# Kernel tuning notes

Hardware: AMD Instinct MI355X
Metric: run time of the kernel (lower is better)

The kernel has to match this reference:

```python
import jax, jax.numpy as jnp
import numpy as np

DIM_IN = 64
DIM_OUT = 64
SCALE = DIM_IN ** (-0.5)

def setup_inputs() -> dict:
    key = jax.random.key(0)
    ks = jax.random.split(key, 9)
    B, C, N, S = 4, DIM_IN, 16384, 16
    inp = {
        "xyz": jax.random.normal(ks[0], (B, 3, N), jnp.float32),
        "neighbor_xyz": jax.random.normal(ks[1], (B, 3, N, S), jnp.float32),
        "point": jax.random.normal(ks[2], (B, C, N), jnp.float32),
        "neighbor_points": jax.random.normal(ks[3], (B, C, N, S), jnp.float32),
        "neighbor_cost": jax.random.normal(ks[4], (B, C, N, S), jnp.float32),
        # 1x1 conv weights (kernel dims squeezed): [out_ch, in_ch]
        "w_k": jax.random.normal(ks[5], (DIM_IN, DIM_IN), jnp.float32) * (DIM_IN ** -0.5),
        "w_v": jax.random.normal(ks[6], (DIM_OUT, DIM_IN), jnp.float32) * (DIM_IN ** -0.5),
        "w_pos": jax.random.normal(ks[7], (DIM_IN, 4), jnp.float32) * 0.5,
        "b_pos": jax.random.normal(ks[8], (DIM_IN,), jnp.float32) * 0.01,
    }
    return inp

def reference(xyz, neighbor_xyz, point, neighbor_points, neighbor_cost, w_k, w_v, w_pos, b_pos):
    # xyz: [B,3,N]; neighbor_xyz: [B,3,N,S]; point: [B,C,N]; neighbor_cost: [B,C,N,S]
    tmp = xyz[:, :, :, None] - neighbor_xyz                      # [B,3,N,S]
    xyz_norm = jnp.linalg.norm(tmp, axis=1, keepdims=True)       # [B,1,N,S]
    pos = jnp.concatenate([tmp, xyz_norm], axis=1)               # [B,4,N,S]
    pos_enc = jnp.einsum('oc,bcns->bons', w_pos, pos) + b_pos[None, :, None, None]
    k = jnp.einsum('oc,bcns->bons', w_k, neighbor_cost + pos_enc)  # [B,C,N,S]
    v = jnp.einsum('oc,bcns->bons', w_v, neighbor_cost)            # [B,Co,N,S]
    q = point * SCALE                                              # note: self.q conv unused in original
    attn = jnp.einsum('bcn,bcns->bns', q, k)                       # channel-reduced scores
    attn = jax.nn.softmax(attn, axis=-1)                           # softmax over S neighbors
    out = jnp.einsum('bns,bcns->bcn', attn, v)                     # [B,Co,N]
    return out
```

## Files before the change

kernel.cpp:

```cpp
#include <hip/hip_runtime.h>

#define NCH    64
#define NPTS   16384
#define NS     16
#define QSCALE 0.125f

__global__ __launch_bounds__(256) void pt_attn_kernel(
    const float* __restrict__ xyz,
    const float* __restrict__ nxyz,
    const float* __restrict__ point,
    const float* __restrict__ cost,
    const float* __restrict__ w_k,
    const float* __restrict__ w_v,
    const float* __restrict__ w_pos,
    const float* __restrict__ b_pos,
    float* __restrict__ out)
{
    __shared__ float ptwc[NCH][64];
    __shared__ float qp[NCH][64];
    __shared__ float qg[5][64];

    const int t  = threadIdx.x;
    const int b  = blockIdx.x >> 8;
    const int n0 = (blockIdx.x & 255) << 6;

    const float* point_b = point + (size_t)b * NCH * NPTS;
    const float* cost_b  = cost  + (size_t)b * NCH * NPTS * NS;
    const float* xyz_b   = xyz   + (size_t)b * 3 * NPTS;
    const float* nxyz_b  = nxyz  + (size_t)b * 3 * NPTS * NS;
    float*       out_b   = out   + (size_t)b * NCH * NPTS;

    const int wu   = __builtin_amdgcn_readfirstlane(t >> 6);
    const int lane = t & 63;

#pragma unroll
    for (int i = 0; i < 4; ++i) {
        int o = wu * 4 + i;
        ptwc[o][lane] = point_b[o * NPTS + n0 + lane] * QSCALE;
    }
#pragma unroll
    for (int i = 4; i < 16; ++i) {
        int o = wu * 4 + (i & 3) + (i >> 2) * 16;
        ptwc[o][lane] = point_b[o * NPTS + n0 + lane] * QSCALE;
    }
    __syncthreads();

    {
        const int cbase = wu * 16;
        float acc[16];
#pragma unroll
        for (int j = 0; j < 16; ++j) acc[j] = 0.f;
#pragma unroll 4
        for (int o = 0; o < NCH; ++o) {
            float pv = ptwc[o][lane];
            const float* wkr = w_k + o * NCH + cbase;
#pragma unroll
            for (int j = 0; j < 16; ++j)
                acc[j] = fmaf(wkr[j], pv, acc[j]);
        }
#pragma unroll
        for (int j = 0; j < 16; ++j)
            qp[cbase + j][lane] = acc[j];
    }
    __syncthreads();

    {
        const int j = wu;
        float a = 0.f, ab = 0.f;
#pragma unroll 8
        for (int c = 0; c < NCH; ++c) {
            float q = qp[c][lane];
            a = fmaf(q, w_pos[c * 4 + j], a);
            if (j == 0) ab = fmaf(q, b_pos[c], ab);
        }
        qg[j][lane] = a;
        if (j == 0) qg[4][lane] = ab;
    }
    __syncthreads();

    const int s4 = t & 3, nl = t >> 2;
    const int n  = n0 + nl;
    const float4* costp = (const float4*)(cost_b + (size_t)n * NS) + s4;

    float4 lg;
    {
        float x0 = xyz_b[0 * NPTS + n];
        float x1 = xyz_b[1 * NPTS + n];
        float x2 = xyz_b[2 * NPTS + n];
        float4 a0 = *(const float4*)(nxyz_b + (size_t)(0 * NPTS + n) * NS + s4 * 4);
        float4 a1 = *(const float4*)(nxyz_b + (size_t)(1 * NPTS + n) * NS + s4 * 4);
        float4 a2 = *(const float4*)(nxyz_b + (size_t)(2 * NPTS + n) * NS + s4 * 4);
        float qs0 = qg[0][nl], qs1 = qg[1][nl], qs2 = qg[2][nl];
        float qs3 = qg[3][nl], qb  = qg[4][nl];
        float t0, t1, t2, nr;
        t0 = x0 - a0.x; t1 = x1 - a1.x; t2 = x2 - a2.x;
        nr = sqrtf(fmaf(t0, t0, fmaf(t1, t1, t2 * t2)));
        lg.x = fmaf(qs0, t0, fmaf(qs1, t1, fmaf(qs2, t2, fmaf(qs3, nr, qb))));
        t0 = x0 - a0.y; t1 = x1 - a1.y; t2 = x2 - a2.y;
        nr = sqrtf(fmaf(t0, t0, fmaf(t1, t1, t2 * t2)));
        lg.y = fmaf(qs0, t0, fmaf(qs1, t1, fmaf(qs2, t2, fmaf(qs3, nr, qb))));
        t0 = x0 - a0.z; t1 = x1 - a1.z; t2 = x2 - a2.z;
        nr = sqrtf(fmaf(t0, t0, fmaf(t1, t1, t2 * t2)));
        lg.z = fmaf(qs0, t0, fmaf(qs1, t1, fmaf(qs2, t2, fmaf(qs3, nr, qb))));
        t0 = x0 - a0.w; t1 = x1 - a1.w; t2 = x2 - a2.w;
        nr = sqrtf(fmaf(t0, t0, fmaf(t1, t1, t2 * t2)));
        lg.w = fmaf(qs0, t0, fmaf(qs1, t1, fmaf(qs2, t2, fmaf(qs3, nr, qb))));
    }

#pragma unroll 8
    for (int c = 0; c < NCH; ++c) {
        float4 cv = costp[(size_t)c * NPTS * 4];
        float qc = qp[c][nl];
        lg.x = fmaf(qc, cv.x, lg.x);
        lg.y = fmaf(qc, cv.y, lg.y);
        lg.z = fmaf(qc, cv.z, lg.z);
        lg.w = fmaf(qc, cv.w, lg.w);
    }

    float m = fmaxf(fmaxf(lg.x, lg.y), fmaxf(lg.z, lg.w));
    m = fmaxf(m, __shfl_xor(m, 1));
    m = fmaxf(m, __shfl_xor(m, 2));
    float4 at;
    at.x = __expf(lg.x - m);
    at.y = __expf(lg.y - m);
    at.z = __expf(lg.z - m);
    at.w = __expf(lg.w - m);
    float Z = at.x + at.y + at.z + at.w;
    Z += __shfl_xor(Z, 1);
    Z += __shfl_xor(Z, 2);
    float rz = 1.f / Z;
    at.x *= rz; at.y *= rz; at.z *= rz; at.w *= rz;

#pragma unroll 8
    for (int c = 0; c < NCH; ++c) {
        float4 cv = costp[(size_t)c * NPTS * 4];
        float p = fmaf(at.x, cv.x, fmaf(at.y, cv.y, fmaf(at.z, cv.z, at.w * cv.w)));
        p += __shfl_xor(p, 1);
        p += __shfl_xor(p, 2);
        if (s4 == 0) ptwc[c][nl] = p;
    }
    __syncthreads();

    {
        const int obase = wu * 16;
        float acc[16];
#pragma unroll
        for (int j = 0; j < 16; ++j) acc[j] = 0.f;
#pragma unroll 4
        for (int c = 0; c < NCH; ++c) {
            float wv = ptwc[c][lane];
            const float* wvc = w_v + c;
#pragma unroll
            for (int j = 0; j < 16; ++j)
                acc[j] = fmaf(wvc[(obase + j) * NCH], wv, acc[j]);
        }
#pragma unroll
        for (int j = 0; j < 16; ++j)
            out_b[(obase + j) * NPTS + n0 + lane] = acc[j];
    }
}

extern "C" void kernel_launch(void* const* d_in, const int* in_sizes, int n_in,
                              void* d_out, int out_size, void* d_ws, size_t ws_size,
                              hipStream_t stream) {
    const float* xyz   = (const float*)d_in[0];
    const float* nxyz  = (const float*)d_in[1];
    const float* point = (const float*)d_in[2];
    const float* cost  = (const float*)d_in[4];
    const float* w_k   = (const float*)d_in[5];
    const float* w_v   = (const float*)d_in[6];
    const float* w_pos = (const float*)d_in[7];
    const float* b_pos = (const float*)d_in[8];
    float* outp = (float*)d_out;

    dim3 grid(1024), block(256);
    hipLaunchKernelGGL(pt_attn_kernel, grid, block, 0, stream,
                       xyz, nxyz, point, cost, w_k, w_v, w_pos, b_pos, outp);
}
```

Measured before the change: 535.2 us.

## Shrink point tile to 16 and cache cost tile in registers

Cuts the per-block point tile from 64 to 16 and launches four times as many blocks. Each thread now loads its share of the cost tensor into registers once and reuses it for both the logit and the weighted-sum passes, where before it read cost from global memory twice. The two weight matrices are staged in padded shared memory and the small channel matvecs use float4 LDS reads. In exchange, every block reloads both full 64x64 weight matrices, syncs more often, and holds 64 extra registers for the cost tile, which could limit occupancy.

After: 498.2 us. -6.9%, faster.

```diff
diff --git a/kernel.cpp b/kernel.cpp
--- a/kernel.cpp
+++ b/kernel.cpp
@@ -5,7 +5,7 @@
 #define NS     16
 #define QSCALE 0.125f
 
-__global__ __launch_bounds__(256) void pt_attn_kernel(
+__global__ __launch_bounds__(256, 4) void pt_attn_kernel(
     const float* __restrict__ xyz,
     const float* __restrict__ nxyz,
     const float* __restrict__ point,
@@ -16,13 +16,17 @@
     const float* __restrict__ b_pos,
     float* __restrict__ out)
 {
-    __shared__ float ptwc[NCH][64];
-    __shared__ float qp[NCH][64];
-    __shared__ float qg[5][64];
+    __shared__ float wmat[64][68];
+    __shared__ float ptq[64][16];
+    __shared__ float qp[16][68];
+    __shared__ float wpb[5][65];
+    __shared__ float qg[5][16];
+    __shared__ float linit[4][64];
+    __shared__ float wc[16][68];
 
     const int t  = threadIdx.x;
-    const int b  = blockIdx.x >> 8;
-    const int n0 = (blockIdx.x & 255) << 6;
+    const int b  = blockIdx.x >> 10;
+    const int n0 = (blockIdx.x & 1023) << 4;
 
     const float* point_b = point + (size_t)b * NCH * NPTS;
     const float* cost_b  = cost  + (size_t)b * NCH * NPTS * NS;
@@ -30,133 +34,145 @@
     const float* nxyz_b  = nxyz  + (size_t)b * 3 * NPTS * NS;
     float*       out_b   = out   + (size_t)b * NCH * NPTS;
 
-    const int wu   = __builtin_amdgcn_readfirstlane(t >> 6);
+    const int w    = __builtin_amdgcn_readfirstlane(t >> 6);
     const int lane = t & 63;
 
 #pragma unroll
-    for (int i = 0; i < 4; ++i) {
-        int o = wu * 4 + i;
-        ptwc[o][lane] = point_b[o * NPTS + n0 + lane] * QSCALE;
+    for (int i = 0; i < 16; ++i) {
+        int idx = t + i * 256;
+        wmat[idx >> 6][idx & 63] = w_k[idx];
     }
 #pragma unroll
-    for (int i = 4; i < 16; ++i) {
-        int o = wu * 4 + (i & 3) + (i >> 2) * 16;
-        ptwc[o][lane] = point_b[o * NPTS + n0 + lane] * QSCALE;
+    for (int i = 0; i < 4; ++i) {
+        int idx = t + i * 256;
+        ptq[idx >> 4][idx & 15] = point_b[(idx >> 4) * NPTS + n0 + (idx & 15)] * QSCALE;
+    }
+    wpb[t & 3][t >> 2] = w_pos[t];
+    if (t < 64) wpb[4][t] = b_pos[t];
+    __syncthreads();
+
+    {
+        const int nl = t & 15, cg = t >> 4;
+        float a0 = 0.f, a1 = 0.f, a2 = 0.f, a3 = 0.f;
+#pragma unroll 8
+        for (int o = 0; o < NCH; ++o) {
+            float pvv = ptq[o][nl];
+            float4 wk = *(const float4*)&wmat[o][cg * 4];
+            a0 = fmaf(wk.x, pvv, a0);
+            a1 = fmaf(wk.y, pvv, a1);
+            a2 = fmaf(wk.z, pvv, a2);
+            a3 = fmaf(wk.w, pvv, a3);
+        }
+        float4 r; r.x = a0; r.y = a1; r.z = a2; r.w = a3;
+        *(float4*)&qp[nl][cg * 4] = r;
     }
     __syncthreads();
 
-    {
-        const int cbase = wu * 16;
-        float acc[16];
+    if (t < 80) {
+        const int j = t >> 4, nl = t & 15;
+        float a = 0.f;
+#pragma unroll 8
+        for (int c = 0; c < NCH; ++c)
+            a = fmaf(qp[nl][c], wpb[j][c], a);
+        qg[j][nl] = a;
+    }
 #pragma unroll
-        for (int j = 0; j < 16; ++j) acc[j] = 0.f;
-#pragma unroll 4
-        for (int o = 0; o < NCH; ++o) {
-            float pv = ptwc[o][lane];
-            const float* wkr = w_k + o * NCH + cbase;
-#pragma unroll
-            for (int j = 0; j < 16; ++j)
-                acc[j] = fmaf(wkr[j], pv, acc[j]);
-        }
-#pragma unroll
-        for (int j = 0; j < 16; ++j)
-            qp[cbase + j][lane] = acc[j];
+    for (int i = 0; i < 16; ++i) {
+        int idx = t + i * 256;
+        wmat[idx & 63][idx >> 6] = w_v[idx];
     }
     __syncthreads();
 
+    const int n0w = n0 + (w << 2);
+    const int c2  = lane >> 4;
+    const int nn  = (lane >> 2) & 3;
+    const int s4  = lane & 3;
+    const int gn  = lane >> 4;
+    const int gs  = lane & 15;
+
+    float gx0 = xyz_b[0 * NPTS + n0w + gn];
+    float gx1 = xyz_b[1 * NPTS + n0w + gn];
+    float gx2 = xyz_b[2 * NPTS + n0w + gn];
+    float ga0 = nxyz_b[(size_t)(0 * NPTS + n0w + gn) * NS + gs];
+    float ga1 = nxyz_b[(size_t)(1 * NPTS + n0w + gn) * NS + gs];
+    float ga2 = nxyz_b[(size_t)(2 * NPTS + n0w + gn) * NS + gs];
+
+    const float4* cbase = (const float4*)(cost_b + (size_t)(n0w + nn) * NS) + s4;
+    float4 cr[16];
+#pragma unroll
+    for (int g = 0; g < 16; ++g)
+        cr[g] = cbase[(size_t)(g * 4 + c2) * NPTS * 4];
+
     {
-        const int j = wu;
-        float a = 0.f, ab = 0.f;
-#pragma unroll 8
-        for (int c = 0; c < NCH; ++c) {
-            float q = qp[c][lane];
-            a = fmaf(q, w_pos[c * 4 + j], a);
-            if (j == 0) ab = fmaf(q, b_pos[c], ab);
-        }
-        qg[j][lane] = a;
-        if (j == 0) qg[4][lane] = ab;
+        float t0 = gx0 - ga0, t1 = gx1 - ga1, t2 = gx2 - ga2;
+        float nr = sqrtf(fmaf(t0, t0, fmaf(t1, t1, t2 * t2)));
+        int nlg = (w << 2) + gn;
+        float li = fmaf(qg[0][nlg], t0, fmaf(qg[1][nlg], t1,
+                   fmaf(qg[2][nlg], t2, fmaf(qg[3][nlg], nr, qg[4][nlg]))));
+        linit[w][lane] = li;
     }
-    __syncthreads();
+    float4 lg = *(const float4*)&linit[w][nn * 16 + s4 * 4];
+    if (c2 != 0) { lg.x = 0.f; lg.y = 0.f; lg.z = 0.f; lg.w = 0.f; }
 
-    const int s4 = t & 3, nl = t >> 2;
-    const int n  = n0 + nl;
-    const float4* costp = (const float4*)(cost_b + (size_t)n * NS) + s4;
-
-    float4 lg;
-    {
-        float x0 = xyz_b[0 * NPTS + n];
-        float x1 = xyz_b[1 * NPTS + n];
-        float x2 = xyz_b[2 * NPTS + n];
-        float4 a0 = *(const float4*)(nxyz_b + (size_t)(0 * NPTS + n) * NS + s4 * 4);
-        float4 a1 = *(const float4*)(nxyz_b + (size_t)(1 * NPTS + n) * NS + s4 * 4);
-        float4 a2 = *(const float4*)(nxyz_b + (size_t)(2 * NPTS + n) * NS + s4 * 4);
-        float qs0 = qg[0][nl], qs1 = qg[1][nl], qs2 = qg[2][nl];
-        float qs3 = qg[3][nl], qb  = qg[4][nl];
-        float t0, t1, t2, nr;
-        t0 = x0 - a0.x; t1 = x1 - a1.x; t2 = x2 - a2.x;
-        nr = sqrtf(fmaf(t0, t0, fmaf(t1, t1, t2 * t2)));
-        lg.x = fmaf(qs0, t0, fmaf(qs1, t1, fmaf(qs2, t2, fmaf(qs3, nr, qb))));
-        t0 = x0 - a0.y; t1 = x1 - a1.y; t2 = x2 - a2.y;
-        nr = sqrtf(fmaf(t0, t0, fmaf(t1, t1, t2 * t2)));
-        lg.y = fmaf(qs0, t0, fmaf(qs1, t1, fmaf(qs2, t2, fmaf(qs3, nr, qb))));
-        t0 = x0 - a0.z; t1 = x1 - a1.z; t2 = x2 - a2.z;
-        nr = sqrtf(fmaf(t0, t0, fmaf(t1, t1, t2 * t2)));
-        lg.z = fmaf(qs0, t0, fmaf(qs1, t1, fmaf(qs2, t2, fmaf(qs3, nr, qb))));
-        t0 = x0 - a0.w; t1 = x1 - a1.w; t2 = x2 - a2.w;
-        nr = sqrtf(fmaf(t0, t0, fmaf(t1, t1, t2 * t2)));
-        lg.w = fmaf(qs0, t0, fmaf(qs1, t1, fmaf(qs2, t2, fmaf(qs3, nr, qb))));
+    const int nl = (w << 2) + nn;
+#pragma unroll
+    for (int g = 0; g < 16; ++g) {
+        float qv = qp[nl][g * 4 + c2];
+        lg.x = fmaf(qv, cr[g].x, lg.x);
+        lg.y = fmaf(qv, cr[g].y, lg.y);
+        lg.z = fmaf(qv, cr[g].z, lg.z);
+        lg.w = fmaf(qv, cr[g].w, lg.w);
     }
-
-#pragma unroll 8
-    for (int c = 0; c < NCH; ++c) {
-        float4 cv = costp[(size_t)c * NPTS * 4];
-        float qc = qp[c][nl];
-        lg.x = fmaf(qc, cv.x, lg.x);
-        lg.y = fmaf(qc, cv.y, lg.y);
-        lg.z = fmaf(qc, cv.z, lg.z);
-        lg.w = fmaf(qc, cv.w, lg.w);
-    }
+    lg.x += __shfl_xor(lg.x, 16); lg.y += __shfl_xor(lg.y, 16);
+    lg.z += __shfl_xor(lg.z, 16); lg.w += __shfl_xor(lg.w, 16);
+    lg.x += __shfl_xor(lg.x, 32); lg.y += __shfl_xor(lg.y, 32);
+    lg.z += __shfl_xor(lg.z, 32); lg.w += __shfl_xor(lg.w, 32);
 
     float m = fmaxf(fmaxf(lg.x, lg.y), fmaxf(lg.z, lg.w));
     m = fmaxf(m, __shfl_xor(m, 1));
     m = fmaxf(m, __shfl_xor(m, 2));
     float4 at;
-    at.x = __expf(lg.x - m);
-    at.y = __expf(lg.y - m);
-    at.z = __expf(lg.z - m);
-    at.w = __expf(lg.w - m);
+    at.x = __expf(lg.x - m); at.y = __expf(lg.y - m);
+    at.z = __expf(lg.z - m); at.w = __expf(lg.w - m);
     float Z = at.x + at.y + at.z + at.w;
     Z += __shfl_xor(Z, 1);
     Z += __shfl_xor(Z, 2);
     float rz = 1.f / Z;
     at.x *= rz; at.y *= rz; at.z *= rz; at.w *= rz;
 
-#pragma unroll 8
-    for (int c = 0; c < NCH; ++c) {
-        float4 cv = costp[(size_t)c * NPTS * 4];
-        float p = fmaf(at.x, cv.x, fmaf(at.y, cv.y, fmaf(at.z, cv.z, at.w * cv.w)));
+    float pv[16];
+#pragma unroll
+    for (int g = 0; g < 16; ++g) {
+        float p = fmaf(at.x, cr[g].x, fmaf(at.y, cr[g].y,
+                  fmaf(at.z, cr[g].z, at.w * cr[g].w)));
         p += __shfl_xor(p, 1);
         p += __shfl_xor(p, 2);
-        if (s4 == 0) ptwc[c][nl] = p;
+        pv[g] = p;
+    }
+    if (s4 == 0) {
+#pragma unroll
+        for (int g = 0; g < 16; ++g)
+            wc[nl][g * 4 + c2] = pv[g];
     }
     __syncthreads();
 
     {
-        const int obase = wu * 16;
-        float acc[16];
-#pragma unroll
-        for (int j = 0; j < 16; ++j) acc[j] = 0.f;
-#pragma unroll 4
+        const int og = t >> 4, nlo = t & 15;
+        float a0 = 0.f, a1 = 0.f, a2 = 0.f, a3 = 0.f;
+#pragma unroll 8
         for (int c = 0; c < NCH; ++c) {
-            float wv = ptwc[c][lane];
-            const float* wvc = w_v + c;
-#pragma unroll
-            for (int j = 0; j < 16; ++j)
-                acc[j] = fmaf(wvc[(obase + j) * NCH], wv, acc[j]);
+            float wcv = wc[nlo][c];
+            float4 wv = *(const float4*)&wmat[c][og * 4];
+            a0 = fmaf(wv.x, wcv, a0);
+            a1 = fmaf(wv.y, wcv, a1);
+            a2 = fmaf(wv.z, wcv, a2);
+            a3 = fmaf(wv.w, wcv, a3);
         }
-#pragma unroll
-        for (int j = 0; j < 16; ++j)
-            out_b[(obase + j) * NPTS + n0 + lane] = acc[j];
+        float* op = out_b + (size_t)(og * 4) * NPTS + n0 + nlo;
+        op[0]        = a0;
+        op[NPTS]     = a1;
+        op[2 * NPTS] = a2;
+        op[3 * NPTS] = a3;
     }
 }
 
@@ -173,7 +189,7 @@
     const float* b_pos = (const float*)d_in[8];
     float* outp = (float*)d_out;
 
-    dim3 grid(1024), block(256);
+    dim3 grid(4096), block(256);
     hipLaunchKernelGGL(pt_attn_kernel, grid, block, 0, stream,
                        xyz, nxyz, point, cost, w_k, w_v, w_pos, b_pos, outp);
 }
```
